# Kernel tuning notes

Measured on AMD Instinct MI355X. Metric: run time of the kernel, lower is better.

## Reference

```python
import jax, jax.numpy as jnp
import numpy as np

NUM_HEADS = 30
EPS = 1e-5


def _fp32_layernorm(x):
    # LayerNorm over last dim, no affine, computed in fp32 (FP32LayerNorm)
    xf = x.astype(jnp.float32)
    mu = jnp.mean(xf, axis=-1, keepdims=True)
    var = jnp.mean(jnp.square(xf - mu), axis=-1, keepdims=True)
    return ((xf - mu) * jax.lax.rsqrt(var + EPS)).astype(x.dtype)


def _apply_rotary(x, cos, sin):
    # x: [B,H,S,hd]; cos/sin: [S,hd] -> broadcast via [None,None]
    half = x.shape[-1] // 2
    xr, xi = x[..., :half], x[..., half:]
    x_rot = jnp.concatenate([-xi, xr], axis=-1)
    out = x.astype(jnp.float32) * cos[None, None] + x_rot.astype(jnp.float32) * sin[None, None]
    return out.astype(x.dtype)


def setup_inputs() -> dict:
    key = jax.random.key(0)
    ks = jax.random.split(key, 12)
    B, S_img, S_txt, D = 1, 3072, 256, 1920
    hd = D // NUM_HEADS
    s = 0.02
    return {
        "hidden_states": jax.random.normal(ks[0], (B, S_img, D), jnp.float32),
        "encoder_hidden_states": jax.random.normal(ks[1], (B, S_txt, D), jnp.float32),
        "rope_cos": jax.random.normal(ks[2], (S_img, hd), jnp.float32),
        "rope_sin": jax.random.normal(ks[3], (S_img, hd), jnp.float32),
        "Wq": jax.random.normal(ks[4], (D, D), jnp.float32) * s,
        "bq": jnp.zeros((D,), jnp.float32),
        "Wk": jax.random.normal(ks[5], (D, D), jnp.float32) * s,
        "bk": jnp.zeros((D,), jnp.float32),
        "Wv": jax.random.normal(ks[6], (D, D), jnp.float32) * s,
        "bv": jnp.zeros((D,), jnp.float32),
        "Wo": jax.random.normal(ks[7], (D, D), jnp.float32) * s,
        "bo": jnp.zeros((D,), jnp.float32),
    }


def reference(hidden_states, encoder_hidden_states, rope_cos, rope_sin,
              Wq, bq, Wk, bk, Wv, bv, Wo, bo):
    T = encoder_hidden_states.shape[1]  # text_seq_length
    x = jnp.concatenate([encoder_hidden_states, hidden_states], axis=1)  # [B,S,D]
    B, S, D = x.shape
    H = NUM_HEADS
    hd = D // H

    def proj(W, b):
        return (x @ W.T + b).reshape(B, S, H, hd).transpose(0, 2, 1, 3)  # [B,H,S,hd]

    q = _fp32_layernorm(proj(Wq, bq))
    k = _fp32_layernorm(proj(Wk, bk))
    v = proj(Wv, bv)

    # partial RoPE: only the image slice (tokens after text)
    q = q.at[:, :, T:, :].set(_apply_rotary(q[:, :, T:, :], rope_cos, rope_sin))
    k = k.at[:, :, T:, :].set(_apply_rotary(k[:, :, T:, :], rope_cos, rope_sin))

    scale = 1.0 / jnp.sqrt(jnp.asarray(hd, q.dtype))
    scores = jnp.einsum("bhqd,bhkd->bhqk", q, k) * scale
    attn = jax.nn.softmax(scores, axis=-1)
    out = jnp.einsum("bhqk,bhkd->bhqd", attn, v)  # [B,H,S,hd]

    out = out.transpose(0, 2, 1, 3).reshape(B, S, D)
    out = out @ Wo.T + bo
    return (out[:, T:], out[:, :T])  # (image hidden_states, encoder_hidden_states)
```

## Files before the change

### kernel.cpp

```cpp
#include <hip/hip_runtime.h>

constexpr int S_TOT  = 3328;
constexpr int S_TXT  = 256;
constexpr int DMODEL = 1920;
constexpr int NHEAD  = 30;
constexpr int HD     = 64;

typedef _Float16 half8 __attribute__((ext_vector_type(8)));
typedef _Float16 half4v __attribute__((ext_vector_type(4)));
typedef float    f32x4 __attribute__((ext_vector_type(4)));
typedef short    bh8   __attribute__((ext_vector_type(8)));

__device__ __forceinline__ f32x4 mfma16h(half8 a, half8 b, f32x4 c) {
    return __builtin_amdgcn_mfma_f32_16x16x32_f16(a, b, c, 0, 0, 0);
}
__device__ __forceinline__ f32x4 mfma16b(bh8 a, bh8 b, f32x4 c) {
    return __builtin_amdgcn_mfma_f32_16x16x32_bf16(a, b, c, 0, 0, 0);
}
__device__ __forceinline__ void gload16(void* lds, const void* g) {
    __builtin_amdgcn_global_load_lds(
        (const __attribute__((address_space(1))) void*)g,
        (__attribute__((address_space(3))) void*)lds, 16, 0, 0);
}

__device__ __forceinline__ unsigned f2u(float x){ union{float f;unsigned u;}c; c.f=x; return c.u; }
__device__ __forceinline__ float u2f(unsigned x){ union{unsigned u;float f;}c; c.u=x; return c.f; }

__device__ __forceinline__ void split8(const float* p, bh8& hi, bh8& lo) {
    float4 f0 = *(const float4*)p;
    float4 f1 = *(const float4*)(p + 4);
    float f[8] = {f0.x, f0.y, f0.z, f0.w, f1.x, f1.y, f1.z, f1.w};
    union { bh8 v; unsigned short u[8]; } H, L;
    #pragma unroll
    for (int e = 0; e < 8; ++e) {
        unsigned ub = f2u(f[e]);
        H.u[e] = (unsigned short)(ub >> 16);
        float r = f[e] - u2f(ub & 0xFFFF0000u);
        L.u[e] = (unsigned short)(f2u(r) >> 16);
    }
    hi = H.v; lo = L.v;
}

__global__ __launch_bounds__(256) void cvt_xwv(
    const float* __restrict__ hid, const float* __restrict__ enc,
    const float* __restrict__ Wv,
    _Float16* __restrict__ xh, _Float16* __restrict__ Wvh)
{
    const int seg = blockIdx.y;
    const float* src; _Float16* dst; int n;
    switch (seg) {
        case 0:  src = enc; dst = xh;                  n = S_TXT * DMODEL;  break;
        case 1:  src = hid; dst = xh + S_TXT * DMODEL; n = 3072 * DMODEL;   break;
        default: src = Wv;  dst = Wvh;                 n = DMODEL * DMODEL; break;
    }
    for (int i = (blockIdx.x * 256 + threadIdx.x) * 4; i < n; i += gridDim.x * 256 * 4) {
        float4 v = *(const float4*)(src + i);
        half4v h = {(_Float16)v.x, (_Float16)v.y, (_Float16)v.z, (_Float16)v.w};
        *(half4v*)(dst + i) = h;
    }
}

__global__ __launch_bounds__(256) void cvt_wo(const float* __restrict__ Wo,
                                              _Float16* __restrict__ Woh)
{
    const int n = DMODEL * DMODEL;
    for (int i = (blockIdx.x * 256 + threadIdx.x) * 4; i < n; i += gridDim.x * 256 * 4) {
        float4 v = *(const float4*)(Wo + i);
        half4v h = {(_Float16)v.x, (_Float16)v.y, (_Float16)v.z, (_Float16)v.w};
        *(half4v*)(Woh + i) = h;
    }
}

__global__ __launch_bounds__(256) void gemm_v(
    const _Float16* __restrict__ xh,
    const _Float16* __restrict__ Wvh,
    const float* __restrict__ bv,
    _Float16* __restrict__ v_hT)
{
    extern __shared__ __attribute__((aligned(16))) char smem[];
    _Float16* As = (_Float16*)smem;
    _Float16* Bs = (_Float16*)(smem + 8192);

    const int tid  = threadIdx.x;
    const int wave = tid >> 6;
    const int lane = tid & 63;
    const int l16  = lane & 15;
    const int quad = lane >> 4;

    const int m0 = blockIdx.x * 128;
    const int n0 = blockIdx.y * 128;
    const int wm = (wave >> 1) * 64;
    const int wn = (wave & 1) * 64;

    const _Float16* gA = xh  + (size_t)(m0 + wave * 32 + (lane >> 2)) * DMODEL + ((lane & 3) << 3);
    const _Float16* gB = Wvh + (size_t)(n0 + wave * 32 + (lane >> 2)) * DMODEL + ((lane & 3) << 3);
    _Float16* lA = As + wave * 32 * 32;
    _Float16* lB = Bs + wave * 32 * 32;

    f32x4 acc[4][4];
    #pragma unroll
    for (int j = 0; j < 4; ++j)
        #pragma unroll
        for (int i = 0; i < 4; ++i) acc[j][i] = (f32x4){0.f, 0.f, 0.f, 0.f};

    for (int k0 = 0; k0 < DMODEL; k0 += 32) {
        __syncthreads();
        gload16(lA,        gA + k0);
        gload16(lA + 512,  gA + 16 * DMODEL + k0);
        gload16(lB,        gB + k0);
        gload16(lB + 512,  gB + 16 * DMODEL + k0);
        __syncthreads();
        half8 af[4], bf[4];
        #pragma unroll
        for (int j = 0; j < 4; ++j)
            af[j] = *(const half8*)(As + (wm + j * 16 + l16) * 32 + quad * 8);
        #pragma unroll
        for (int i = 0; i < 4; ++i)
            bf[i] = *(const half8*)(Bs + (wn + i * 16 + l16) * 32 + quad * 8);
        #pragma unroll
        for (int j = 0; j < 4; ++j)
            #pragma unroll
            for (int i = 0; i < 4; ++i)
                acc[j][i] = mfma16h(af[j], bf[i], acc[j][i]);
    }
    __syncthreads();

    const int h = (n0 + wn) / 64;
    _Float16* vt = (_Float16*)smem + wave * 64 * 72;
    #pragma unroll
    for (int j = 0; j < 4; ++j)
        #pragma unroll
        for (int r = 0; r < 4; ++r)
            #pragma unroll
            for (int i = 0; i < 4; ++i)
                vt[(i * 16 + l16) * 72 + j * 16 + quad * 4 + r] =
                    (_Float16)(acc[j][i][r] + bv[n0 + wn + i * 16 + l16]);
    __asm__ volatile("" ::: "memory");
    const int dl = lane >> 3;
    const int sl = (lane & 7) << 3;
    #pragma unroll
    for (int t = 0; t < 8; ++t) {
        const int d = t * 8 + dl;
        half8 vv = *(const half8*)(vt + d * 72 + sl);
        *(half8*)(v_hT + (size_t)(h * HD + d) * S_TOT + m0 + wm + sl) = vv;
    }
}

__global__ __launch_bounds__(256) void gemm_qk(
    const float* __restrict__ hid, const float* __restrict__ enc,
    const float* __restrict__ Wq, const float* __restrict__ Wk,
    const float* __restrict__ bq, const float* __restrict__ bk,
    const float* __restrict__ rcos, const float* __restrict__ rsin,
    _Float16* __restrict__ q_h, _Float16* __restrict__ k_h,
    _Float16* __restrict__ q_lo, _Float16* __restrict__ k_lo)
{
    extern __shared__ __attribute__((aligned(16))) char smem[];
    float* As = (float*)smem;
    float* Bs = (float*)(smem + 16384);

    const int tid  = threadIdx.x;
    const int wave = tid >> 6;
    const int lane = tid & 63;
    const int l16  = lane & 15;
    const int quad = lane >> 4;

    const int m0  = blockIdx.x * 128;
    const int n0g = blockIdx.y * 128;
    const int zz  = (n0g >= DMODEL);
    const int nloc = n0g - zz * DMODEL;
    const int wm = (wave >> 1) * 64;
    const int wn = (wave & 1) * 64;

    const float* aSrc = (m0 < S_TXT) ? (enc + (size_t)m0 * DMODEL)
                                     : (hid + (size_t)(m0 - S_TXT) * DMODEL);
    const float* bSrc = (zz ? Wk : Wq) + (size_t)nloc * DMODEL;

    const float* gA = aSrc + (size_t)(wave * 32 + (lane >> 3)) * DMODEL + ((lane & 7) << 2);
    const float* gB = bSrc + (size_t)(wave * 32 + (lane >> 3)) * DMODEL + ((lane & 7) << 2);
    float* lA = As + wave * 32 * 32;
    float* lB = Bs + wave * 32 * 32;

    f32x4 acc[4][4];
    #pragma unroll
    for (int j = 0; j < 4; ++j)
        #pragma unroll
        for (int i = 0; i < 4; ++i) acc[j][i] = (f32x4){0.f, 0.f, 0.f, 0.f};

    for (int k0 = 0; k0 < DMODEL; k0 += 32) {
        __syncthreads();
        #pragma unroll
        for (int t = 0; t < 4; ++t) {
            gload16(lA + t * 256, gA + (size_t)(t * 8) * DMODEL + k0);
            gload16(lB + t * 256, gB + (size_t)(t * 8) * DMODEL + k0);
        }
        __syncthreads();
        bh8 ah[4], al[4], bhv[4], blv[4];
        #pragma unroll
        for (int j = 0; j < 4; ++j)
            split8(As + (wm + j * 16 + l16) * 32 + quad * 8, ah[j], al[j]);
        #pragma unroll
        for (int i = 0; i < 4; ++i)
            split8(Bs + (wn + i * 16 + l16) * 32 + quad * 8, bhv[i], blv[i]);
        #pragma unroll
        for (int j = 0; j < 4; ++j)
            #pragma unroll
            for (int i = 0; i < 4; ++i) {
                acc[j][i] = mfma16b(ah[j], bhv[i], acc[j][i]);
                acc[j][i] = mfma16b(al[j], bhv[i], acc[j][i]);
                acc[j][i] = mfma16b(ah[j], blv[i], acc[j][i]);
            }
    }

    const int h = (nloc + wn) / 64;
    const float* bias = zz ? bk : bq;
    _Float16* dhi = zz ? k_h : q_h;
    _Float16* dlo = zz ? k_lo : q_lo;
    const float qscale = zz ? 1.f : 0.125f;
    const bool rope = (m0 >= S_TXT);

    #pragma unroll
    for (int j = 0; j < 4; ++j) {
        #pragma unroll
        for (int r = 0; r < 4; ++r) {
            const int s = m0 + wm + j * 16 + quad * 4 + r;
            float x[4], s1 = 0.f, s2 = 0.f;
            #pragma unroll
            for (int i = 0; i < 4; ++i) {
                x[i] = acc[j][i][r] + bias[nloc + wn + i * 16 + l16];
                s1 += x[i];
                s2 += x[i] * x[i];
            }
            #pragma unroll
            for (int off = 1; off <= 8; off <<= 1) {
                s1 += __shfl_xor(s1, off);
                s2 += __shfl_xor(s2, off);
            }
            const float mu   = s1 * (1.f / 64.f);
            const float var  = fmaxf(s2 * (1.f / 64.f) - mu * mu, 0.f);
            const float rstd = rsqrtf(var + 1e-5f);
            float xn[4];
            #pragma unroll
            for (int i = 0; i < 4; ++i) xn[i] = (x[i] - mu) * rstd;
            float o[4];
            if (rope) {
                const int pos = s - S_TXT;
                #pragma unroll
                for (int i = 0; i < 4; ++i) {
                    const int d = i * 16 + l16;
                    const float c  = rcos[(size_t)pos * HD + d];
                    const float si = rsin[(size_t)pos * HD + d];
                    const float rot = (i < 2) ? -xn[i ^ 2] : xn[i ^ 2];
                    o[i] = xn[i] * c + rot * si;
                }
            } else {
                #pragma unroll
                for (int i = 0; i < 4; ++i) o[i] = xn[i];
            }
            #pragma unroll
            for (int i = 0; i < 4; ++i) {
                const float vv = o[i] * qscale;
                const _Float16 hv = (_Float16)vv;
                const size_t idx = (size_t)(h * S_TOT + s) * HD + i * 16 + l16;
                dhi[idx] = hv;
                dlo[idx] = (_Float16)((vv - (float)hv) * 1024.f);
            }
        }
    }
}

__global__ __launch_bounds__(256, 2) void attn(
    const _Float16* __restrict__ q_h,  const _Float16* __restrict__ q_lo,
    const _Float16* __restrict__ k_h,  const _Float16* __restrict__ k_lo,
    const _Float16* __restrict__ v_hT,
    _Float16* __restrict__ aout)
{
    extern __shared__ __attribute__((aligned(16))) char smem[];
    _Float16* KsB  = (_Float16*)smem;
    _Float16* KslB = (_Float16*)(smem + 16384);
    _Float16* VsB  = (_Float16*)(smem + 32768);
    _Float16* Pl   = (_Float16*)(smem + 49152);

    const int tid  = threadIdx.x;
    const int wave = tid >> 6;
    const int lane = tid & 63;
    const int l16  = lane & 15;
    const int quad = lane >> 4;
    const int h  = blockIdx.y;
    const int q0 = blockIdx.x * 128 + wave * 32;

    const _Float16* qbase  = q_h  + (size_t)(h * S_TOT + q0) * HD;
    const _Float16* qlbase = q_lo + (size_t)(h * S_TOT + q0) * HD;
    half8 aq0[2], aq1[2], aql0[2], aql1[2];
    #pragma unroll
    for (int j = 0; j < 2; ++j) {
        aq0[j]  = *(const half8*)(qbase  + (j * 16 + l16) * HD + quad * 8);
        aq1[j]  = *(const half8*)(qbase  + (j * 16 + l16) * HD + 32 + quad * 8);
        aql0[j] = *(const half8*)(qlbase + (j * 16 + l16) * HD + quad * 8);
        aql1[j] = *(const half8*)(qlbase + (j * 16 + l16) * HD + 32 + quad * 8);
    }

    const _Float16* kbase  = k_h  + (size_t)h * S_TOT * HD;
    const _Float16* klbase = k_lo + (size_t)h * S_TOT * HD;
    const _Float16* vbase  = v_hT + (size_t)h * HD * S_TOT;

    const int srow = lane >> 3;
    const int schk = ((lane & 7) ^ srow) << 3;
    const _Float16* gK  = kbase  + (size_t)(wave * 16 + srow) * HD + schk;
    const _Float16* gKl = klbase + (size_t)(wave * 16 + srow) * HD + schk;
    const _Float16* gV  = vbase  + (size_t)(wave * 16 + srow) * S_TOT + schk;

    const int c0 = (quad ^ (l16 & 7)) << 3;
    const int c1 = c0 ^ 32;

    f32x4 o[2][4];
    float m_i[2][4], l_i[2][4];
    #pragma unroll
    for (int j = 0; j < 2; ++j)
        #pragma unroll
        for (int i = 0; i < 4; ++i) {
            o[j][i] = (f32x4){0.f, 0.f, 0.f, 0.f};
            m_i[j][i] = -1e30f; l_i[j][i] = 0.f;
        }

    constexpr int NT = S_TOT / 64;

    auto stage = [&](int kv0, int p) {
        _Float16* lK  = KsB  + p * 4096 + wave * 1024;
        _Float16* lKl = KslB + p * 4096 + wave * 1024;
        _Float16* lV  = VsB  + p * 4096 + wave * 1024;
        gload16(lK,        gK  + (size_t)kv0 * HD);
        gload16(lK + 512,  gK  + (size_t)(kv0 + 8) * HD);
        gload16(lKl,       gKl + (size_t)kv0 * HD);
        gload16(lKl + 512, gKl + (size_t)(kv0 + 8) * HD);
        gload16(lV,        gV + kv0);
        gload16(lV + 512,  gV + kv0 + 8 * S_TOT);
    };

    stage(0, 0);
    for (int t = 0; t < NT; ++t) {
        const int cur = t & 1;
        if (t + 1 < NT) {
            stage((t + 1) * 64, cur ^ 1);
            asm volatile("s_waitcnt vmcnt(6)" ::: "memory");
        } else {
            asm volatile("s_waitcnt vmcnt(0)" ::: "memory");
        }
        __builtin_amdgcn_s_barrier();
        const _Float16* Ks  = KsB  + cur * 4096;
        const _Float16* Ksl = KslB + cur * 4096;
        const _Float16* Vs  = VsB  + cur * 4096;

        f32x4 sc[2][4];
        #pragma unroll
        for (int i = 0; i < 4; ++i) {
            const int rb = (i * 16 + l16) * 64;
            half8 b0 = *(const half8*)(Ks  + rb + c0);
            half8 b1 = *(const half8*)(Ks  + rb + c1);
            half8 d0 = *(const half8*)(Ksl + rb + c0);
            half8 d1 = *(const half8*)(Ksl + rb + c1);
            #pragma unroll
            for (int j = 0; j < 2; ++j) {
                f32x4 s  = (f32x4){0.f, 0.f, 0.f, 0.f};
                f32x4 s2 = (f32x4){0.f, 0.f, 0.f, 0.f};
                s  = mfma16h(aq0[j],  b0, s);   s  = mfma16h(aq1[j],  b1, s);
                s2 = mfma16h(aql0[j], b0, s2);  s2 = mfma16h(aql1[j], b1, s2);
                s2 = mfma16h(aq0[j],  d0, s2);  s2 = mfma16h(aq1[j],  d1, s2);
                sc[j][i] = s + s2 * 0.0009765625f;
            }
        }
        #pragma unroll
        for (int j = 0; j < 2; ++j)
            #pragma unroll
            for (int r = 0; r < 4; ++r) {
                float mx = fmaxf(fmaxf(sc[j][0][r], sc[j][1][r]),
                                 fmaxf(sc[j][2][r], sc[j][3][r]));
                mx = fmaxf(mx, __shfl_xor(mx, 1));
                mx = fmaxf(mx, __shfl_xor(mx, 2));
                mx = fmaxf(mx, __shfl_xor(mx, 4));
                mx = fmaxf(mx, __shfl_xor(mx, 8));
                const float mnew  = fmaxf(m_i[j][r], mx);
                const float alpha = __expf(m_i[j][r] - mnew);
                m_i[j][r] = mnew;
                float rs = 0.f;
                #pragma unroll
                for (int i = 0; i < 4; ++i) {
                    float p = __expf(sc[j][i][r] - mnew);
                    rs += p;
                    Pl[(wave * 32 + j * 16 + quad * 4 + r) * 72 + i * 16 + l16] = (_Float16)p;
                }
                l_i[j][r] = l_i[j][r] * alpha + rs;
                #pragma unroll
                for (int i = 0; i < 4; ++i) o[j][i][r] *= alpha;
            }
        __asm__ volatile("" ::: "memory");
        half8 ap0[2], ap1[2];
        #pragma unroll
        for (int j = 0; j < 2; ++j) {
            ap0[j] = *(const half8*)(Pl + (wave * 32 + j * 16 + l16) * 72 + quad * 8);
            ap1[j] = *(const half8*)(Pl + (wave * 32 + j * 16 + l16) * 72 + 32 + quad * 8);
        }
        #pragma unroll
        for (int i = 0; i < 4; ++i) {
            const int rb = (i * 16 + l16) * 64;
            half8 vb0 = *(const half8*)(Vs + rb + c0);
            half8 vb1 = *(const half8*)(Vs + rb + c1);
            #pragma unroll
            for (int j = 0; j < 2; ++j) {
                o[j][i] = mfma16h(ap0[j], vb0, o[j][i]);
                o[j][i] = mfma16h(ap1[j], vb1, o[j][i]);
            }
        }
        __builtin_amdgcn_s_barrier();
    }
    #pragma unroll
    for (int j = 0; j < 2; ++j)
        #pragma unroll
        for (int r = 0; r < 4; ++r) {
            float l = l_i[j][r];
            l += __shfl_xor(l, 1);
            l += __shfl_xor(l, 2);
            l += __shfl_xor(l, 4);
            l += __shfl_xor(l, 8);
            const float inv = 1.f / l;
            const int srow2 = q0 + j * 16 + quad * 4 + r;
            #pragma unroll
            for (int i = 0; i < 4; ++i)
                aout[(size_t)srow2 * DMODEL + h * HD + i * 16 + l16] =
                    (_Float16)(o[j][i][r] * inv);
        }
}

__global__ __launch_bounds__(256) void gemm_out(
    const _Float16* __restrict__ A,
    const _Float16* __restrict__ Woh,
    const float* __restrict__ bo,
    float* __restrict__ out)
{
    extern __shared__ __attribute__((aligned(16))) char smem[];
    _Float16* As = (_Float16*)smem;
    _Float16* Bs = (_Float16*)(smem + 8192);

    const int tid  = threadIdx.x;
    const int wave = tid >> 6;
    const int lane = tid & 63;
    const int l16  = lane & 15;
    const int quad = lane >> 4;

    const int m0 = blockIdx.x * 128;
    const int n0 = blockIdx.y * 128;
    const int wm = (wave >> 1) * 64;
    const int wn = (wave & 1) * 64;

    const _Float16* gA = A   + (size_t)(m0 + wave * 32 + (lane >> 2)) * DMODEL + ((lane & 3) << 3);
    const _Float16* gB = Woh + (size_t)(n0 + wave * 32 + (lane >> 2)) * DMODEL + ((lane & 3) << 3);
    _Float16* lA = As + wave * 32 * 32;
    _Float16* lB = Bs + wave * 32 * 32;

    f32x4 acc[4][4];
    #pragma unroll
    for (int j = 0; j < 4; ++j)
        #pragma unroll
        for (int i = 0; i < 4; ++i) acc[j][i] = (f32x4){0.f, 0.f, 0.f, 0.f};

    for (int k0 = 0; k0 < DMODEL; k0 += 32) {
        __syncthreads();
        gload16(lA,        gA + k0);
        gload16(lA + 512,  gA + 16 * DMODEL + k0);
        gload16(lB,        gB + k0);
        gload16(lB + 512,  gB + 16 * DMODEL + k0);
        __syncthreads();
        half8 af[4], bf[4];
        #pragma unroll
        for (int j = 0; j < 4; ++j)
            af[j] = *(const half8*)(As + (wm + j * 16 + l16) * 32 + quad * 8);
        #pragma unroll
        for (int i = 0; i < 4; ++i)
            bf[i] = *(const half8*)(Bs + (wn + i * 16 + l16) * 32 + quad * 8);
        #pragma unroll
        for (int j = 0; j < 4; ++j)
            #pragma unroll
            for (int i = 0; i < 4; ++i)
                acc[j][i] = mfma16h(af[j], bf[i], acc[j][i]);
    }
    #pragma unroll
    for (int j = 0; j < 4; ++j) {
        #pragma unroll
        for (int i = 0; i < 4; ++i) {
            const int n = n0 + wn + i * 16 + l16;
            const float bb = bo[n];
            #pragma unroll
            for (int r = 0; r < 4; ++r) {
                const int m = m0 + wm + j * 16 + quad * 4 + r;
                const int orow = (m >= S_TXT) ? (m - S_TXT) : (m + 3072);
                out[(size_t)orow * DMODEL + n] = acc[j][i][r] + bb;
            }
        }
    }
}

extern "C" void kernel_launch(void* const* d_in, const int* in_sizes, int n_in,
                              void* d_out, int out_size, void* d_ws, size_t ws_size,
                              hipStream_t stream) {
    const float* hid  = (const float*)d_in[0];
    const float* enc  = (const float*)d_in[1];
    const float* rcos = (const float*)d_in[2];
    const float* rsin = (const float*)d_in[3];
    const float* Wq   = (const float*)d_in[4];
    const float* bq   = (const float*)d_in[5];
    const float* Wk   = (const float*)d_in[6];
    const float* bk   = (const float*)d_in[7];
    const float* Wv   = (const float*)d_in[8];
    const float* bv   = (const float*)d_in[9];
    const float* Wo   = (const float*)d_in[10];
    const float* bo   = (const float*)d_in[11];

    char* ws = (char*)d_ws;
    _Float16* xh   = (_Float16*)(ws + 0);
    _Float16* aout = (_Float16*)(ws + 0);
    _Float16* q_h  = (_Float16*)(ws + 12779520);
    _Float16* Woh  = (_Float16*)(ws + 12779520);
    _Float16* k_h  = (_Float16*)(ws + 25559040);
    _Float16* v_hT = (_Float16*)(ws + 38338560);
    _Float16* Wvh  = (_Float16*)d_out;
    _Float16* q_lo = (_Float16*)d_out;
    _Float16* k_lo = (_Float16*)((char*)d_out + 12779520);

    static bool attn_attr_set = false;
    if (!attn_attr_set) {
        (void)hipFuncSetAttribute(reinterpret_cast<const void*>(&attn),
                                  hipFuncAttributeMaxDynamicSharedMemorySize, 67584);
        attn_attr_set = true;
    }

    cvt_xwv<<<dim3(128, 3), 256, 0, stream>>>(hid, enc, Wv, xh, Wvh);
    gemm_v<<<dim3(26, 15), 256, 36864, stream>>>(xh, Wvh, bv, v_hT);
    gemm_qk<<<dim3(26, 30), 256, 32768, stream>>>(
        hid, enc, Wq, Wk, bq, bk, rcos, rsin, q_h, k_h, q_lo, k_lo);
    attn<<<dim3(26, NHEAD), 256, 67584, stream>>>(q_h, q_lo, k_h, k_lo, v_hT, aout);
    cvt_wo<<<dim3(128), 256, 0, stream>>>(Wo, Woh);
    gemm_out<<<dim3(26, 15), 256, 16384, stream>>>(aout, Woh, bo, (float*)d_out);
}
```

Before: 850.8 us.

## Single-buffer V and shrink P scratch in attention to fit three blocks per CU

```diff
diff --git a/kernel.cpp b/kernel.cpp
--- a/kernel.cpp
+++ b/kernel.cpp
@@ -25,6 +25,10 @@
 
 __device__ __forceinline__ unsigned f2u(float x){ union{float f;unsigned u;}c; c.f=x; return c.u; }
 __device__ __forceinline__ float u2f(unsigned x){ union{unsigned u;float f;}c; c.u=x; return c.f; }
+
+#define MAXDPP(v, ctrl)                                                        \
+    v = fmaxf(v, u2f(__builtin_amdgcn_update_dpp(                              \
+            (int)f2u(v), (int)f2u(v), (ctrl), 0xf, 0xf, false)))
 
 __device__ __forceinline__ void split8(const float* p, bh8& hi, bh8& lo) {
     float4 f0 = *(const float4*)p;
@@ -268,7 +272,7 @@
     }
 }
 
-__global__ __launch_bounds__(256, 2) void attn(
+__global__ __launch_bounds__(256, 3) void attn(
     const _Float16* __restrict__ q_h,  const _Float16* __restrict__ q_lo,
     const _Float16* __restrict__ k_h,  const _Float16* __restrict__ k_lo,
     const _Float16* __restrict__ v_hT,
@@ -277,8 +281,8 @@
     extern __shared__ __attribute__((aligned(16))) char smem[];
     _Float16* KsB  = (_Float16*)smem;
     _Float16* KslB = (_Float16*)(smem + 16384);
-    _Float16* VsB  = (_Float16*)(smem + 32768);
-    _Float16* Pl   = (_Float16*)(smem + 49152);
+    _Float16* Vs   = (_Float16*)(smem + 32768);
+    _Float16* Pl   = (_Float16*)(smem + 40960);
 
     const int tid  = threadIdx.x;
     const int wave = tid >> 6;
@@ -324,31 +328,33 @@
 
     constexpr int NT = S_TOT / 64;
 
-    auto stage = [&](int kv0, int p) {
+    auto stageK = [&](int kv0, int p) {
         _Float16* lK  = KsB  + p * 4096 + wave * 1024;
         _Float16* lKl = KslB + p * 4096 + wave * 1024;
-        _Float16* lV  = VsB  + p * 4096 + wave * 1024;
         gload16(lK,        gK  + (size_t)kv0 * HD);
         gload16(lK + 512,  gK  + (size_t)(kv0 + 8) * HD);
         gload16(lKl,       gKl + (size_t)kv0 * HD);
         gload16(lKl + 512, gKl + (size_t)(kv0 + 8) * HD);
-        gload16(lV,        gV + kv0);
-        gload16(lV + 512,  gV + kv0 + 8 * S_TOT);
     };
-
-    stage(0, 0);
+    auto stageV = [&](int kv0) {
+        _Float16* lV = Vs + wave * 1024;
+        gload16(lV,       gV + kv0);
+        gload16(lV + 512, gV + kv0 + 8 * S_TOT);
+    };
+
+    stageK(0, 0);
+    stageV(0);
     for (int t = 0; t < NT; ++t) {
         const int cur = t & 1;
         if (t + 1 < NT) {
-            stage((t + 1) * 64, cur ^ 1);
+            stageK((t + 1) * 64, cur ^ 1);
             asm volatile("s_waitcnt vmcnt(6)" ::: "memory");
         } else {
-            asm volatile("s_waitcnt vmcnt(0)" ::: "memory");
+            asm volatile("s_waitcnt vmcnt(2)" ::: "memory");
         }
         __builtin_amdgcn_s_barrier();
         const _Float16* Ks  = KsB  + cur * 4096;
         const _Float16* Ksl = KslB + cur * 4096;
-        const _Float16* Vs  = VsB  + cur * 4096;
 
         f32x4 sc[2][4];
         #pragma unroll
@@ -368,16 +374,17 @@
                 sc[j][i] = s + s2 * 0.0009765625f;
             }
         }
-        #pragma unroll
-        for (int j = 0; j < 2; ++j)
+        half8 ap0[2], ap1[2];
+        #pragma unroll
+        for (int j = 0; j < 2; ++j) {
             #pragma unroll
             for (int r = 0; r < 4; ++r) {
                 float mx = fmaxf(fmaxf(sc[j][0][r], sc[j][1][r]),
                                  fmaxf(sc[j][2][r], sc[j][3][r]));
-                mx = fmaxf(mx, __shfl_xor(mx, 1));
-                mx = fmaxf(mx, __shfl_xor(mx, 2));
-                mx = fmaxf(mx, __shfl_xor(mx, 4));
-                mx = fmaxf(mx, __shfl_xor(mx, 8));
+                MAXDPP(mx, 0xB1);
+                MAXDPP(mx, 0x4E);
+                MAXDPP(mx, 0x124);
+                MAXDPP(mx, 0x128);
                 const float mnew  = fmaxf(m_i[j][r], mx);
                 const float alpha = __expf(m_i[j][r] - mnew);
                 m_i[j][r] = mnew;
@@ -386,19 +393,20 @@
                 for (int i = 0; i < 4; ++i) {
                     float p = __expf(sc[j][i][r] - mnew);
                     rs += p;
-                    Pl[(wave * 32 + j * 16 + quad * 4 + r) * 72 + i * 16 + l16] = (_Float16)p;
+                    Pl[(wave * 16 + quad * 4 + r) * 72 + i * 16 + l16] = (_Float16)p;
                 }
                 l_i[j][r] = l_i[j][r] * alpha + rs;
                 #pragma unroll
                 for (int i = 0; i < 4; ++i) o[j][i][r] *= alpha;
             }
-        __asm__ volatile("" ::: "memory");
-        half8 ap0[2], ap1[2];
-        #pragma unroll
-        for (int j = 0; j < 2; ++j) {
-            ap0[j] = *(const half8*)(Pl + (wave * 32 + j * 16 + l16) * 72 + quad * 8);
-            ap1[j] = *(const half8*)(Pl + (wave * 32 + j * 16 + l16) * 72 + 32 + quad * 8);
-        }
+            __asm__ volatile("" ::: "memory");
+            ap0[j] = *(const half8*)(Pl + (wave * 16 + l16) * 72 + quad * 8);
+            ap1[j] = *(const half8*)(Pl + (wave * 16 + l16) * 72 + 32 + quad * 8);
+            __asm__ volatile("" ::: "memory");
+        }
+        if (t + 1 < NT) asm volatile("s_waitcnt vmcnt(4)" ::: "memory");
+        else            asm volatile("s_waitcnt vmcnt(0)" ::: "memory");
+        __builtin_amdgcn_s_barrier();
         #pragma unroll
         for (int i = 0; i < 4; ++i) {
             const int rb = (i * 16 + l16) * 64;
@@ -410,7 +418,9 @@
                 o[j][i] = mfma16h(ap1[j], vb1, o[j][i]);
             }
         }
+        asm volatile("s_waitcnt lgkmcnt(0)" ::: "memory");
         __builtin_amdgcn_s_barrier();
+        if (t + 1 < NT) stageV((t + 1) * 64);
     }
     #pragma unroll
     for (int j = 0; j < 2; ++j)
@@ -525,18 +535,11 @@
     _Float16* q_lo = (_Float16*)d_out;
     _Float16* k_lo = (_Float16*)((char*)d_out + 12779520);
 
-    static bool attn_attr_set = false;
-    if (!attn_attr_set) {
-        (void)hipFuncSetAttribute(reinterpret_cast<const void*>(&attn),
-                                  hipFuncAttributeMaxDynamicSharedMemorySize, 67584);
-        attn_attr_set = true;
-    }
-
     cvt_xwv<<<dim3(128, 3), 256, 0, stream>>>(hid, enc, Wv, xh, Wvh);
     gemm_v<<<dim3(26, 15), 256, 36864, stream>>>(xh, Wvh, bv, v_hT);
     gemm_qk<<<dim3(26, 30), 256, 32768, stream>>>(
         hid, enc, Wq, Wk, bq, bk, rcos, rsin, q_h, k_h, q_lo, k_lo);
-    attn<<<dim3(26, NHEAD), 256, 67584, stream>>>(q_h, q_lo, k_h, k_lo, v_hT, aout);
+    attn<<<dim3(26, NHEAD), 256, 50176, stream>>>(q_h, q_lo, k_h, k_lo, v_hT, aout);
     cvt_wo<<<dim3(128), 256, 0, stream>>>(Wo, Woh);
     gemm_out<<<dim3(26, 15), 256, 16384, stream>>>(aout, Woh, bo, (float*)d_out);
 }
```

Measured after the change: 783.6 us. -7.9%, faster.
